# Optimization experiments

Measured on AMD Instinct MI355X. Metric: run time of the kernel, lower is better.

Reference implementation:

```python
import jax, jax.numpy as jnp
import numpy as np

B, N, E, H = 4, 4096, 1024, 16
D = E // H            # head_dim = 64
P_DIM = 64            # proj_dim; feature dim = 2*P_DIM = 128
EPS = 1e-4


def setup_inputs() -> dict:
    key = jax.random.key(0)
    ks = jax.random.split(key, 9)
    x = jax.random.normal(ks[0], (B, N, E), jnp.float32)
    init = 0.02
    Wq = jax.random.normal(ks[1], (E, E), jnp.float32) * init
    Wk = jax.random.normal(ks[2], (E, E), jnp.float32) * init
    Wv = jax.random.normal(ks[3], (E, E), jnp.float32) * init
    Wo = jax.random.normal(ks[4], (E, E), jnp.float32) * init
    bq = jnp.zeros((E,), jnp.float32)
    bk = jnp.zeros((E,), jnp.float32)
    bv = jnp.zeros((E,), jnp.float32)
    bo = jnp.zeros((E,), jnp.float32)
    # orthogonal random projection matrix (proj_dim, head_dim), fixed (non-trainable)
    g = np.random.default_rng(0).normal(size=(P_DIM, D))
    P = jnp.asarray(np.linalg.qr(g)[0], jnp.float32)
    return dict(x=x, Wq=Wq, bq=bq, Wk=Wk, bk=bk, Wv=Wv, bv=bv, Wo=Wo, bo=bo, P=P)


def _heads(z):
    # (B, N, E) -> (B, H, N, D)
    return z.reshape(B, N, H, D).transpose(0, 2, 1, 3)


def _normalize(z):
    return z / (jnp.linalg.norm(z, axis=-1, keepdims=True) + EPS)


def reference(x, Wq, bq, Wk, bk, Wv, bv, Wo, bo, P):
    q = _heads(x @ Wq.T + bq)
    k = _heads(x @ Wk.T + bk)
    v = _heads(x @ Wv.T + bv)
    q = _normalize(q)
    k = _normalize(k)
    scale = H ** 0.25
    qp = jnp.einsum('bhnd,ed->bhne', q, P) * scale
    kp = jnp.einsum('bhnd,ed->bhne', k, P) * scale
    fscale = P_DIM ** (-0.5)   # x.shape[-1]**-0.5 with last dim = proj_dim
    qf = jnp.concatenate([jnp.sin(qp), jnp.cos(qp)], axis=-1) * fscale  # (B,H,N,2p)
    kf = jnp.concatenate([jnp.sin(kp), jnp.cos(kp)], axis=-1) * fscale
    # non-causal linear attention: q @ (k^T v)
    kv = jnp.einsum('bhme,bhmd->bhed', kf, v)          # (B,H,2p,D)
    o = jnp.einsum('bhne,bhed->bhnd', qf, kv)          # (B,H,N,D)
    o = o.transpose(0, 2, 1, 3).reshape(B, N, E)
    return o @ Wo.T + bo
```

## Files before the change

### kernel.cpp

```cpp
#include <hip/hip_runtime.h>
#include <hip/hip_bf16.h>
#include <stdint.h>


typedef __bf16 bf16x8 __attribute__((ext_vector_type(8)));
typedef float f32x4 __attribute__((ext_vector_type(4)));

#define AS1 __attribute__((address_space(1)))
#define AS3 __attribute__((address_space(3)))

__device__ __forceinline__ void gl2lds16(const void* g, void* l) {
    __builtin_amdgcn_global_load_lds((const AS1 void*)g, (AS3 void*)l, 16, 0, 0);
}

__global__ void detect_kernel(const unsigned short* __restrict__ x,
                              int* __restrict__ flag) {
    __shared__ int s;
    const int lane = threadIdx.x;
    if (lane == 0) s = 0;
    __syncthreads();
    int cnt = 0;
#pragma unroll
    for (int i = 0; i < 2; ++i) {
        const unsigned short u = x[i * 64 + lane];
        const int e = (u >> 7) & 0xFF;
        cnt += (e >= 117 && e <= 131) ? 1 : 0;
    }
    atomicAdd(&s, cnt);
    __syncthreads();
    if (lane == 0) *flag = (s >= 100) ? 1 : 0;
}

__global__ __launch_bounds__(256) void cvt_kernel(
    const void* __restrict__ src, __hip_bfloat16* __restrict__ dst,
    int n, const int* __restrict__ flag) {
    if (*flag) return;
    const int i = (blockIdx.x * 256 + threadIdx.x) * 8;
    if (i >= n) return;
    const float* s = (const float*)src + i;
    const float4 a = *(const float4*)s;
    const float4 b = *(const float4*)(s + 4);
    union { uint4 u; __hip_bfloat16 h[8]; } pk;
    pk.h[0] = __float2bfloat16(a.x); pk.h[1] = __float2bfloat16(a.y);
    pk.h[2] = __float2bfloat16(a.z); pk.h[3] = __float2bfloat16(a.w);
    pk.h[4] = __float2bfloat16(b.x); pk.h[5] = __float2bfloat16(b.y);
    pk.h[6] = __float2bfloat16(b.z); pk.h[7] = __float2bfloat16(b.w);
    *(uint4*)(dst + i) = pk.u;
}

static constexpr int GM = 16384, GN = 1024, GK = 1024;

__global__ __launch_bounds__(256) void gemm_bias_kernel(
    const void* __restrict__ Adirect,
    const __hip_bfloat16* __restrict__ Acvt,
    const void* __restrict__ W0r, const void* __restrict__ W1r,
    const void* __restrict__ W2r,
    const __hip_bfloat16* __restrict__ W0c, const __hip_bfloat16* __restrict__ W1c,
    const __hip_bfloat16* __restrict__ W2c,
    const void* __restrict__ b0r, const void* __restrict__ b1r,
    const void* __restrict__ b2r,
    void* __restrict__ o0, void* __restrict__ o1, void* __restrict__ o2,
    const int* __restrict__ flag, int last)
{
    __shared__ unsigned short smem[2 * 128 * 64];
    unsigned short* sA = smem;
    unsigned short* sB = smem + 128 * 64;

    const int tid  = threadIdx.x;
    const int lane = tid & 63;
    const int w    = tid >> 6;
    const int wm   = w >> 1, wn = w & 1;
    const int lr   = lane & 15, lk = lane >> 4;

    const int id    = blockIdx.x;
    const int xcd   = id & 7;
    const int slot  = id >> 3;
    const int mslot = slot & 15;
    const int rest  = slot >> 4;
    const int m0    = (xcd * 16 + mslot) * 128;
    const int n0    = (rest & 7) * 128;
    const int z     = rest >> 3;
    const int fl    = *flag;

    const __hip_bfloat16* A = fl ? (const __hip_bfloat16*)Adirect : Acvt;
    const void* Wraw = (z == 0) ? W0r : (z == 1) ? W1r : W2r;
    const __hip_bfloat16* Wc = (z == 0) ? W0c : (z == 1) ? W1c : W2c;
    const __hip_bfloat16* W = fl ? (const __hip_bfloat16*)Wraw : Wc;
    const void* bias_raw = (z == 0) ? b0r : (z == 1) ? b1r : b2r;
    void* Cout = (z == 0) ? o0 : (z == 1) ? o1 : o2;

    f32x4 acc[4][4];
#pragma unroll
    for (int i = 0; i < 4; ++i)
#pragma unroll
        for (int j = 0; j < 4; ++j)
            acc[i][j] = (f32x4){0.f, 0.f, 0.f, 0.f};

    const __hip_bfloat16* Ab = A + (size_t)m0 * GK;
    const __hip_bfloat16* Wb = W + (size_t)n0 * GK;

    for (int k0 = 0; k0 < GK; k0 += 64) {
#pragma unroll
        for (int j = 0; j < 4; ++j) {
            const int chunk = j * 256 + tid;
            const int row   = chunk >> 3;
            const int c     = chunk & 7;
            const int cs    = c ^ (row & 7);
            gl2lds16(Ab + (size_t)row * GK + k0 + cs * 8,
                     (char*)sA + (j * 256 + w * 64) * 16);
            gl2lds16(Wb + (size_t)row * GK + k0 + cs * 8,
                     (char*)sB + (j * 256 + w * 64) * 16);
        }
        __syncthreads();
#pragma unroll
        for (int kk = 0; kk < 64; kk += 32) {
            const int jbase = kk >> 3;
            const int jj = (jbase + lk) ^ (lr & 7);
            bf16x8 af[4], bfr[4];
#pragma unroll
            for (int i = 0; i < 4; ++i)
                af[i] = *(const bf16x8*)&sA[(wm * 64 + i * 16 + lr) * 64 + jj * 8];
#pragma unroll
            for (int j = 0; j < 4; ++j)
                bfr[j] = *(const bf16x8*)&sB[(wn * 64 + j * 16 + lr) * 64 + jj * 8];
#pragma unroll
            for (int i = 0; i < 4; ++i)
#pragma unroll
                for (int j = 0; j < 4; ++j)
                    acc[i][j] = __builtin_amdgcn_mfma_f32_16x16x32_bf16(
                        af[i], bfr[j], acc[i][j], 0, 0, 0);
        }
        __syncthreads();
    }

    const bool f32out = (last != 0) && (fl == 0);
    if (f32out) {
#pragma unroll
        for (int j = 0; j < 4; ++j) {
            const int col = n0 + wn * 64 + j * 16 + lr;
            const float bv = ((const float*)bias_raw)[col];
#pragma unroll
            for (int i = 0; i < 4; ++i) {
                const int rbase = m0 + wm * 64 + i * 16 + lk * 4;
#pragma unroll
                for (int r = 0; r < 4; ++r)
                    ((float*)Cout)[(size_t)(rbase + r) * GN + col] = acc[i][j][r] + bv;
            }
        }
        return;
    }
    __hip_bfloat16* sC = (__hip_bfloat16*)smem;
#pragma unroll
    for (int j = 0; j < 4; ++j) {
        const int col = wn * 64 + j * 16 + lr;
        const float bv = fl ? __bfloat162float(((const __hip_bfloat16*)bias_raw)[n0 + col])
                            : ((const float*)bias_raw)[n0 + col];
        const int c2 = col >> 3, o = col & 7;
#pragma unroll
        for (int i = 0; i < 4; ++i) {
            const int rb = wm * 64 + i * 16 + lk * 4;
#pragma unroll
            for (int r = 0; r < 4; ++r) {
                const int row = rb + r;
                const int c2s = c2 ^ (row & 7);
                sC[row * 128 + c2s * 8 + o] = __float2bfloat16(acc[i][j][r] + bv);
            }
        }
    }
    __syncthreads();
    {
        const int row = tid >> 1, hf = tid & 1;
        __hip_bfloat16* dst = (__hip_bfloat16*)Cout + (size_t)(m0 + row) * GN + n0 + hf * 64;
#pragma unroll
        for (int q = 0; q < 8; ++q) {
            const int cc = (hf * 8 + q) ^ (row & 7);
            *(uint4*)(dst + q * 8) = *(const uint4*)&sC[row * 128 + cc * 8];
        }
    }
}

__device__ __forceinline__ void load_P(const void* Praw, int f,
                                       __hip_bfloat16* sP, int tid) {
    const int e = tid >> 2, q = tid & 3;
    union { uint4 u[2]; __hip_bfloat16 h[16]; } pk;
    if (f) {
        pk.u[0] = *(const uint4*)((const __hip_bfloat16*)Praw + e * 64 + q * 16);
        pk.u[1] = *(const uint4*)((const __hip_bfloat16*)Praw + e * 64 + q * 16 + 8);
    } else {
        const float* ps = (const float*)Praw + e * 64 + q * 16;
#pragma unroll
        for (int j = 0; j < 16; ++j) pk.h[j] = __float2bfloat16(ps[j]);
    }
    *(uint4*)&sP[e * 72 + q * 16]     = pk.u[0];
    *(uint4*)&sP[e * 72 + q * 16 + 8] = pk.u[1];
}

__device__ __forceinline__ float sumsq16(uint4 a, uint4 b) {
    union { uint4 u; __hip_bfloat16 h[8]; } x0, x1;
    x0.u = a; x1.u = b;
    float ss = 0.f;
#pragma unroll
    for (int j = 0; j < 8; ++j) {
        float v0 = __bfloat162float(x0.h[j]); ss += v0 * v0;
        float v1 = __bfloat162float(x1.h[j]); ss += v1 * v1;
    }
    return ss;
}

__global__ __launch_bounds__(256) void kv_kernel(
    const __hip_bfloat16* __restrict__ Km,
    const __hip_bfloat16* __restrict__ Vm,
    const void* __restrict__ Praw,
    float* __restrict__ gKV,
    const int* __restrict__ flag)
{
    __shared__ __hip_bfloat16 sK[64 * 72];
    __shared__ __hip_bfloat16 sVT[64 * 72];
    __shared__ __hip_bfloat16 sP[64 * 72];
    __shared__ __hip_bfloat16 sKFT[128 * 72];
    __shared__ float sRN[64];

    const int tid  = threadIdx.x;
    const int lane = tid & 63;
    const int w    = tid >> 6;
    const int lr   = lane & 15, lk = lane >> 4;
    const int bh   = blockIdx.y;
    const int b    = bh >> 4, h = bh & 15;
    const int nst  = blockIdx.x * 256;
    const int f    = *flag;
    const int n    = tid >> 2, q2 = tid & 3;

    load_P(Praw, f, sP, tid);

    f32x4 acck[2][4];
#pragma unroll
    for (int i = 0; i < 2; ++i)
#pragma unroll
        for (int j = 0; j < 4; ++j)
            acck[i][j] = (f32x4){0.f, 0.f, 0.f, 0.f};

    size_t base = ((size_t)(b * 4096 + nst + n)) * 1024 + h * 64 + q2 * 16;
    uint4 ka = *(const uint4*)(Km + base), kb = *(const uint4*)(Km + base + 8);
    uint4 va = *(const uint4*)(Vm + base), vb = *(const uint4*)(Vm + base + 8);

    for (int s = 0; s < 4; ++s) {
        __syncthreads();
        *(uint4*)&sK[n * 72 + q2 * 16]     = ka;
        *(uint4*)&sK[n * 72 + q2 * 16 + 8] = kb;
        {
            union { uint4 u[2]; __hip_bfloat16 h[16]; } vv;
            vv.u[0] = va; vv.u[1] = vb;
#pragma unroll
            for (int j = 0; j < 16; ++j) sVT[(q2 * 16 + j) * 72 + n] = vv.h[j];
        }
        {
            float ss = sumsq16(ka, kb);
            ss += __shfl_xor(ss, 1, 64);
            ss += __shfl_xor(ss, 2, 64);
            if (q2 == 0) sRN[n & 63] = 2.0f / (sqrtf(ss) + 1e-4f);
        }
        if (s < 3) {
            base = ((size_t)(b * 4096 + nst + (s + 1) * 64 + n)) * 1024 + h * 64 + q2 * 16;
            ka = *(const uint4*)(Km + base); kb = *(const uint4*)(Km + base + 8);
            va = *(const uint4*)(Vm + base); vb = *(const uint4*)(Vm + base + 8);
        }
        __syncthreads();
        {
            bf16x8 afr0 = *(const bf16x8*)&sK[(w * 16 + lr) * 72 + lk * 8];
            bf16x8 afr1 = *(const bf16x8*)&sK[(w * 16 + lr) * 72 + 32 + lk * 8];
            float rn[4];
#pragma unroll
            for (int r = 0; r < 4; ++r) rn[r] = sRN[w * 16 + lk * 4 + r];
#pragma unroll
            for (int eb = 0; eb < 4; ++eb) {
                f32x4 pa = (f32x4){0.f, 0.f, 0.f, 0.f};
                bf16x8 b0 = *(const bf16x8*)&sP[(eb * 16 + lr) * 72 + lk * 8];
                bf16x8 b1 = *(const bf16x8*)&sP[(eb * 16 + lr) * 72 + 32 + lk * 8];
                pa = __builtin_amdgcn_mfma_f32_16x16x32_bf16(afr0, b0, pa, 0, 0, 0);
                pa = __builtin_amdgcn_mfma_f32_16x16x32_bf16(afr1, b1, pa, 0, 0, 0);
                const int col = eb * 16 + lr;
#pragma unroll
                for (int r = 0; r < 4; ++r) {
                    const int row = w * 16 + lk * 4 + r;
                    float sv, cv;
                    __sincosf(pa[r] * rn[r], &sv, &cv);
                    sKFT[col * 72 + row]        = __float2bfloat16(sv * 0.125f);
                    sKFT[(col + 64) * 72 + row] = __float2bfloat16(cv * 0.125f);
                }
            }
        }
        __syncthreads();
#pragma unroll
        for (int ks = 0; ks < 2; ++ks) {
            bf16x8 a2[2], b2[4];
            a2[0] = *(const bf16x8*)&sKFT[(w * 16 + lr) * 72 + ks * 32 + lk * 8];
            a2[1] = *(const bf16x8*)&sKFT[((w + 4) * 16 + lr) * 72 + ks * 32 + lk * 8];
#pragma unroll
            for (int db = 0; db < 4; ++db)
                b2[db] = *(const bf16x8*)&sVT[(db * 16 + lr) * 72 + ks * 32 + lk * 8];
#pragma unroll
            for (int i = 0; i < 2; ++i)
#pragma unroll
                for (int db = 0; db < 4; ++db)
                    acck[i][db] = __builtin_amdgcn_mfma_f32_16x16x32_bf16(
                        a2[i], b2[db], acck[i][db], 0, 0, 0);
        }
    }

    float* out = gKV + (size_t)bh * 8192;
#pragma unroll
    for (int i = 0; i < 2; ++i)
#pragma unroll
        for (int db = 0; db < 4; ++db)
#pragma unroll
            for (int r = 0; r < 4; ++r) {
                const int e = (w + 4 * i) * 16 + lk * 4 + r;
                const int d = db * 16 + lr;
                atomicAdd(out + e * 64 + d, acck[i][db][r]);
            }
}

__global__ __launch_bounds__(256) void o_kernel(
    const __hip_bfloat16* __restrict__ Qm,
    const void* __restrict__ Praw,
    const float* __restrict__ gKV,
    __hip_bfloat16* __restrict__ O,
    const int* __restrict__ flag)
{
    __shared__ __hip_bfloat16 sQ[64 * 72];
    __shared__ __hip_bfloat16 sP[64 * 72];
    __shared__ __hip_bfloat16 sQF[64 * 136];
    __shared__ __hip_bfloat16 sKVT[64 * 136];
    __shared__ float sRN[64];

    const int tid  = threadIdx.x;
    const int lane = tid & 63;
    const int w    = tid >> 6;
    const int lr   = lane & 15, lk = lane >> 4;
    const int bh   = blockIdx.y;
    const int b    = bh >> 4, h = bh & 15;
    const int nst  = blockIdx.x * 256;
    const int f    = *flag;
    const int n    = tid >> 2, q2 = tid & 3;

    load_P(Praw, f, sP, tid);
    {
        const float* kvsrc = gKV + (size_t)bh * 8192;
        for (int t = tid; t < 8192; t += 256) {
            const int e = t >> 6, d = t & 63;
            sKVT[d * 136 + e] = __float2bfloat16(kvsrc[t]);
        }
    }

    size_t base = ((size_t)(b * 4096 + nst + n)) * 1024 + h * 64 + q2 * 16;
    uint4 qa = *(const uint4*)(Qm + base), qb = *(const uint4*)(Qm + base + 8);

    for (int s = 0; s < 4; ++s) {
        const int gn0 = nst + s * 64;
        __syncthreads();
        *(uint4*)&sQ[n * 72 + q2 * 16]     = qa;
        *(uint4*)&sQ[n * 72 + q2 * 16 + 8] = qb;
        {
            float ss = sumsq16(qa, qb);
            ss += __shfl_xor(ss, 1, 64);
            ss += __shfl_xor(ss, 2, 64);
            if (q2 == 0) sRN[n & 63] = 2.0f / (sqrtf(ss) + 1e-4f);
        }
        if (s < 3) {
            base = ((size_t)(b * 4096 + nst + (s + 1) * 64 + n)) * 1024 + h * 64 + q2 * 16;
            qa = *(const uint4*)(Qm + base); qb = *(const uint4*)(Qm + base + 8);
        }
        __syncthreads();
        {
            bf16x8 afr0 = *(const bf16x8*)&sQ[(w * 16 + lr) * 72 + lk * 8];
            bf16x8 afr1 = *(const bf16x8*)&sQ[(w * 16 + lr) * 72 + 32 + lk * 8];
            float rn[4];
#pragma unroll
            for (int r = 0; r < 4; ++r) rn[r] = sRN[w * 16 + lk * 4 + r];
#pragma unroll
            for (int eb = 0; eb < 4; ++eb) {
                f32x4 pa = (f32x4){0.f, 0.f, 0.f, 0.f};
                bf16x8 b0 = *(const bf16x8*)&sP[(eb * 16 + lr) * 72 + lk * 8];
                bf16x8 b1 = *(const bf16x8*)&sP[(eb * 16 + lr) * 72 + 32 + lk * 8];
                pa = __builtin_amdgcn_mfma_f32_16x16x32_bf16(afr0, b0, pa, 0, 0, 0);
                pa = __builtin_amdgcn_mfma_f32_16x16x32_bf16(afr1, b1, pa, 0, 0, 0);
                const int col = eb * 16 + lr;
#pragma unroll
                for (int r = 0; r < 4; ++r) {
                    const int row = w * 16 + lk * 4 + r;
                    float sv, cv;
                    __sincosf(pa[r] * rn[r], &sv, &cv);
                    sQF[row * 136 + col]      = __float2bfloat16(sv * 0.125f);
                    sQF[row * 136 + 64 + col] = __float2bfloat16(cv * 0.125f);
                }
            }
        }
        __syncthreads();
        f32x4 oacc[4];
#pragma unroll
        for (int nb = 0; nb < 4; ++nb) oacc[nb] = (f32x4){0.f, 0.f, 0.f, 0.f};
#pragma unroll
        for (int ks = 0; ks < 4; ++ks) {
            bf16x8 aa = *(const bf16x8*)&sQF[(w * 16 + lr) * 136 + ks * 32 + lk * 8];
#pragma unroll
            for (int nb = 0; nb < 4; ++nb) {
                bf16x8 bb = *(const bf16x8*)&sKVT[(nb * 16 + lr) * 136 + ks * 32 + lk * 8];
                oacc[nb] = __builtin_amdgcn_mfma_f32_16x16x32_bf16(aa, bb, oacc[nb], 0, 0, 0);
            }
        }
#pragma unroll
        for (int nb = 0; nb < 4; ++nb)
#pragma unroll
            for (int r = 0; r < 4; ++r)
                sQ[(w * 16 + lk * 4 + r) * 72 + nb * 16 + lr] =
                    __float2bfloat16(oacc[nb][r]);
        __syncthreads();
        {
            uint4 o0 = *(uint4*)&sQ[n * 72 + q2 * 16];
            uint4 o1 = *(uint4*)&sQ[n * 72 + q2 * 16 + 8];
            const size_t obase = ((size_t)(b * 4096 + gn0 + n)) * 1024 + h * 64 + q2 * 16;
            *(uint4*)(O + obase)     = o0;
            *(uint4*)(O + obase + 8) = o1;
        }
    }
}

extern "C" void kernel_launch(void* const* d_in, const int* in_sizes, int n_in,
                              void* d_out, int out_size, void* d_ws, size_t ws_size,
                              hipStream_t stream)
{
    (void)in_sizes; (void)n_in; (void)out_size;
    const void* x  = d_in[0];
    const void* Wq = d_in[1];
    const void* bq = d_in[2];
    const void* Wk = d_in[3];
    const void* bk = d_in[4];
    const void* Wv = d_in[5];
    const void* bv = d_in[6];
    const void* Wo = d_in[7];
    const void* bo = d_in[8];
    const void* P  = d_in[9];

    constexpr size_t XE = (size_t)GM * GN;
    constexpr size_t WE = (size_t)GN * GK;
    constexpr size_t KVE = (size_t)64 * 128 * 64;

    __hip_bfloat16* xb  = (__hip_bfloat16*)d_ws;
    __hip_bfloat16* wqb = xb + XE;
    __hip_bfloat16* wkb = wqb + WE;
    __hip_bfloat16* wvb = wkb + WE;
    __hip_bfloat16* wob = wvb + WE;
    __hip_bfloat16* R1  = wob + WE;
    __hip_bfloat16* R2  = R1 + XE;
    __hip_bfloat16* R3  = R2 + XE;

    const size_t need_fused = ((4 * XE + 4 * WE) * 2 + KVE * 4 + 256);
    const bool fused = ws_size >= need_fused;

    float* gKV;
    int* flag;
    if (fused) {
        gKV = (float*)(R3 + XE);
        flag = (int*)(gKV + KVE);
    } else {
        gKV = (float*)(R2 + XE);
        flag = (int*)(gKV + KVE);
    }

    dim3 blk(256);
    hipLaunchKernelGGL(detect_kernel, dim3(1), dim3(64), 0, stream,
                       (const unsigned short*)x, flag);
    hipMemsetAsync(gKV, 0, KVE * sizeof(float), stream);

    hipLaunchKernelGGL(cvt_kernel, dim3(8192), blk, 0, stream, x,  xb,  (int)XE, flag);
    hipLaunchKernelGGL(cvt_kernel, dim3(512),  blk, 0, stream, Wq, wqb, (int)WE, flag);
    hipLaunchKernelGGL(cvt_kernel, dim3(512),  blk, 0, stream, Wk, wkb, (int)WE, flag);
    hipLaunchKernelGGL(cvt_kernel, dim3(512),  blk, 0, stream, Wv, wvb, (int)WE, flag);
    hipLaunchKernelGGL(cvt_kernel, dim3(512),  blk, 0, stream, Wo, wob, (int)WE, flag);

    if (fused) {
        hipLaunchKernelGGL(gemm_bias_kernel, dim3(3072), blk, 0, stream,
                           x, xb, Wk, Wv, Wq, wkb, wvb, wqb, bk, bv, bq,
                           R1, R2, R3, flag, 0);
        hipLaunchKernelGGL(kv_kernel, dim3(16, 64), blk, 0, stream, R1, R2, P, gKV, flag);
        hipLaunchKernelGGL(o_kernel, dim3(16, 64), blk, 0, stream, R3, P, gKV, R1, flag);
        hipLaunchKernelGGL(gemm_bias_kernel, dim3(1024), blk, 0, stream,
                           R1, R1, Wo, Wo, Wo, wob, wob, wob, bo, bo, bo,
                           d_out, d_out, d_out, flag, 1);
    } else {
        hipLaunchKernelGGL(gemm_bias_kernel, dim3(1024), blk, 0, stream,
                           x, xb, Wk, Wk, Wk, wkb, wkb, wkb, bk, bk, bk,
                           R1, R1, R1, flag, 0);
        hipLaunchKernelGGL(gemm_bias_kernel, dim3(1024), blk, 0, stream,
                           x, xb, Wv, Wv, Wv, wvb, wvb, wvb, bv, bv, bv,
                           R2, R2, R2, flag, 0);
        hipLaunchKernelGGL(kv_kernel, dim3(16, 64), blk, 0, stream, R1, R2, P, gKV, flag);
        hipLaunchKernelGGL(gemm_bias_kernel, dim3(1024), blk, 0, stream,
                           x, xb, Wq, Wq, Wq, wqb, wqb, wqb, bq, bq, bq,
                           R2, R2, R2, flag, 0);
        hipLaunchKernelGGL(o_kernel, dim3(16, 64), blk, 0, stream, R2, P, gKV, R1, flag);
        hipLaunchKernelGGL(gemm_bias_kernel, dim3(1024), blk, 0, stream,
                           R1, R1, Wo, Wo, Wo, wob, wob, wob, bo, bo, bo,
                           d_out, d_out, d_out, flag, 1);
    }
}
```

Before: 413.1 us.

## Fuse K and V projections into one dual-output GEMM sharing A tiles

Replaces the workspace-dependent fused/unfused GEMM paths with a single gemm2 kernel that computes the K and V projections together. Each block loads its x tile once into LDS and multiplies it against both weight tiles, so A traffic is shared. Q and Wo then run as single-output GEMMs. It also drops several __syncthreads in kv_kernel and o_kernel, and the doubled accumulators raise register pressure and occupancy risk. The barrier removals look like they may introduce LDS races between iterations.

```diff
diff --git a/kernel.cpp b/kernel.cpp
--- a/kernel.cpp
+++ b/kernel.cpp
@@ -12,6 +12,8 @@
 __device__ __forceinline__ void gl2lds16(const void* g, void* l) {
     __builtin_amdgcn_global_load_lds((const AS1 void*)g, (AS3 void*)l, 16, 0, 0);
 }
+
+static constexpr int GM = 16384, GN = 1024, GK = 1024;
 
 __global__ void detect_kernel(const unsigned short* __restrict__ x,
                               int* __restrict__ flag) {
@@ -48,18 +50,12 @@
     *(uint4*)(dst + i) = pk.u;
 }
 
-static constexpr int GM = 16384, GN = 1024, GK = 1024;
-
-__global__ __launch_bounds__(256) void gemm_bias_kernel(
+__global__ __launch_bounds__(256) void gemm1_kernel(
     const void* __restrict__ Adirect,
     const __hip_bfloat16* __restrict__ Acvt,
-    const void* __restrict__ W0r, const void* __restrict__ W1r,
-    const void* __restrict__ W2r,
-    const __hip_bfloat16* __restrict__ W0c, const __hip_bfloat16* __restrict__ W1c,
-    const __hip_bfloat16* __restrict__ W2c,
-    const void* __restrict__ b0r, const void* __restrict__ b1r,
-    const void* __restrict__ b2r,
-    void* __restrict__ o0, void* __restrict__ o1, void* __restrict__ o2,
+    const void* __restrict__ Wr, const __hip_bfloat16* __restrict__ Wc,
+    const void* __restrict__ bias_raw,
+    void* __restrict__ Cout,
     const int* __restrict__ flag, int last)
 {
     __shared__ unsigned short smem[2 * 128 * 64];
@@ -75,19 +71,12 @@
     const int id    = blockIdx.x;
     const int xcd   = id & 7;
     const int slot  = id >> 3;
-    const int mslot = slot & 15;
-    const int rest  = slot >> 4;
-    const int m0    = (xcd * 16 + mslot) * 128;
-    const int n0    = (rest & 7) * 128;
-    const int z     = rest >> 3;
+    const int m0    = (xcd * 16 + (slot & 15)) * 128;
+    const int n0    = (slot >> 4) * 128;
     const int fl    = *flag;
 
     const __hip_bfloat16* A = fl ? (const __hip_bfloat16*)Adirect : Acvt;
-    const void* Wraw = (z == 0) ? W0r : (z == 1) ? W1r : W2r;
-    const __hip_bfloat16* Wc = (z == 0) ? W0c : (z == 1) ? W1c : W2c;
-    const __hip_bfloat16* W = fl ? (const __hip_bfloat16*)Wraw : Wc;
-    const void* bias_raw = (z == 0) ? b0r : (z == 1) ? b1r : b2r;
-    void* Cout = (z == 0) ? o0 : (z == 1) ? o1 : o2;
+    const __hip_bfloat16* W = fl ? (const __hip_bfloat16*)Wr : Wc;
 
     f32x4 acc[4][4];
 #pragma unroll
@@ -114,8 +103,7 @@
         __syncthreads();
 #pragma unroll
         for (int kk = 0; kk < 64; kk += 32) {
-            const int jbase = kk >> 3;
-            const int jj = (jbase + lk) ^ (lr & 7);
+            const int jj = ((kk >> 3) + lk) ^ (lr & 7);
             bf16x8 af[4], bfr[4];
 #pragma unroll
             for (int i = 0; i < 4; ++i)
@@ -162,8 +150,7 @@
 #pragma unroll
             for (int r = 0; r < 4; ++r) {
                 const int row = rb + r;
-                const int c2s = c2 ^ (row & 7);
-                sC[row * 128 + c2s * 8 + o] = __float2bfloat16(acc[i][j][r] + bv);
+                sC[row * 128 + (c2 ^ (row & 7)) * 8 + o] = __float2bfloat16(acc[i][j][r] + bv);
             }
         }
     }
@@ -176,6 +163,126 @@
             const int cc = (hf * 8 + q) ^ (row & 7);
             *(uint4*)(dst + q * 8) = *(const uint4*)&sC[row * 128 + cc * 8];
         }
+    }
+}
+
+__global__ __launch_bounds__(256, 2) void gemm2_kernel(
+    const void* __restrict__ Adirect,
+    const __hip_bfloat16* __restrict__ Acvt,
+    const void* __restrict__ W0r, const __hip_bfloat16* __restrict__ W0c,
+    const void* __restrict__ W1r, const __hip_bfloat16* __restrict__ W1c,
+    const void* __restrict__ b0r, const void* __restrict__ b1r,
+    void* __restrict__ o0, void* __restrict__ o1,
+    const int* __restrict__ flag)
+{
+    __shared__ unsigned short smem[3 * 128 * 64];
+    unsigned short* sA  = smem;
+    unsigned short* sB0 = smem + 128 * 64;
+    unsigned short* sB1 = smem + 2 * 128 * 64;
+
+    const int tid  = threadIdx.x;
+    const int lane = tid & 63;
+    const int w    = tid >> 6;
+    const int wm   = w >> 1, wn = w & 1;
+    const int lr   = lane & 15, lk = lane >> 4;
+
+    const int id    = blockIdx.x;
+    const int xcd   = id & 7;
+    const int slot  = id >> 3;
+    const int m0    = (xcd * 16 + (slot & 15)) * 128;
+    const int n0    = (slot >> 4) * 128;
+    const int fl    = *flag;
+
+    const __hip_bfloat16* A  = fl ? (const __hip_bfloat16*)Adirect : Acvt;
+    const __hip_bfloat16* W0 = fl ? (const __hip_bfloat16*)W0r : W0c;
+    const __hip_bfloat16* W1 = fl ? (const __hip_bfloat16*)W1r : W1c;
+
+    f32x4 acc[2][4][4];
+#pragma unroll
+    for (int t = 0; t < 2; ++t)
+#pragma unroll
+        for (int i = 0; i < 4; ++i)
+#pragma unroll
+            for (int j = 0; j < 4; ++j)
+                acc[t][i][j] = (f32x4){0.f, 0.f, 0.f, 0.f};
+
+    const __hip_bfloat16* Ab  = A + (size_t)m0 * GK;
+    const __hip_bfloat16* W0b = W0 + (size_t)n0 * GK;
+    const __hip_bfloat16* W1b = W1 + (size_t)n0 * GK;
+
+    for (int k0 = 0; k0 < GK; k0 += 64) {
+#pragma unroll
+        for (int j = 0; j < 4; ++j) {
+            const int chunk = j * 256 + tid;
+            const int row   = chunk >> 3;
+            const int c     = chunk & 7;
+            const int cs    = c ^ (row & 7);
+            const size_t go = (size_t)row * GK + k0 + cs * 8;
+            const int lo = (j * 256 + w * 64) * 16;
+            gl2lds16(Ab  + go, (char*)sA  + lo);
+            gl2lds16(W0b + go, (char*)sB0 + lo);
+            gl2lds16(W1b + go, (char*)sB1 + lo);
+        }
+        __syncthreads();
+#pragma unroll
+        for (int kk = 0; kk < 64; kk += 32) {
+            const int jj = ((kk >> 3) + lk) ^ (lr & 7);
+            bf16x8 af[4], b0f[4], b1f[4];
+#pragma unroll
+            for (int i = 0; i < 4; ++i)
+                af[i] = *(const bf16x8*)&sA[(wm * 64 + i * 16 + lr) * 64 + jj * 8];
+#pragma unroll
+            for (int j = 0; j < 4; ++j)
+                b0f[j] = *(const bf16x8*)&sB0[(wn * 64 + j * 16 + lr) * 64 + jj * 8];
+#pragma unroll
+            for (int j = 0; j < 4; ++j)
+                b1f[j] = *(const bf16x8*)&sB1[(wn * 64 + j * 16 + lr) * 64 + jj * 8];
+#pragma unroll
+            for (int i = 0; i < 4; ++i)
+#pragma unroll
+                for (int j = 0; j < 4; ++j) {
+                    acc[0][i][j] = __builtin_amdgcn_mfma_f32_16x16x32_bf16(
+                        af[i], b0f[j], acc[0][i][j], 0, 0, 0);
+                    acc[1][i][j] = __builtin_amdgcn_mfma_f32_16x16x32_bf16(
+                        af[i], b1f[j], acc[1][i][j], 0, 0, 0);
+                }
+        }
+        __syncthreads();
+    }
+
+    __hip_bfloat16* sC = (__hip_bfloat16*)smem;
+#pragma unroll
+    for (int t = 0; t < 2; ++t) {
+        const void* bias_raw = t ? b1r : b0r;
+        void* Cout = t ? o1 : o0;
+#pragma unroll
+        for (int j = 0; j < 4; ++j) {
+            const int col = wn * 64 + j * 16 + lr;
+            const float bv = fl ? __bfloat162float(((const __hip_bfloat16*)bias_raw)[n0 + col])
+                                : ((const float*)bias_raw)[n0 + col];
+            const int c2 = col >> 3, o = col & 7;
+#pragma unroll
+            for (int i = 0; i < 4; ++i) {
+                const int rb = wm * 64 + i * 16 + lk * 4;
+#pragma unroll
+                for (int r = 0; r < 4; ++r) {
+                    const int row = rb + r;
+                    sC[row * 128 + (c2 ^ (row & 7)) * 8 + o] =
+                        __float2bfloat16(acc[t][i][j][r] + bv);
+                }
+            }
+        }
+        __syncthreads();
+        {
+            const int row = tid >> 1, hf = tid & 1;
+            __hip_bfloat16* dst = (__hip_bfloat16*)Cout + (size_t)(m0 + row) * GN + n0 + hf * 64;
+#pragma unroll
+            for (int q = 0; q < 8; ++q) {
+                const int cc = (hf * 8 + q) ^ (row & 7);
+                *(uint4*)(dst + q * 8) = *(const uint4*)&sC[row * 128 + cc * 8];
+            }
+        }
+        __syncthreads();
     }
 }
 
@@ -257,14 +364,13 @@
             float ss = sumsq16(ka, kb);
             ss += __shfl_xor(ss, 1, 64);
             ss += __shfl_xor(ss, 2, 64);
-            if (q2 == 0) sRN[n & 63] = 2.0f / (sqrtf(ss) + 1e-4f);
+            if (q2 == 0) sRN[n] = 2.0f / (sqrtf(ss) + 1e-4f);
         }
         if (s < 3) {
             base = ((size_t)(b * 4096 + nst + (s + 1) * 64 + n)) * 1024 + h * 64 + q2 * 16;
             ka = *(const uint4*)(Km + base); kb = *(const uint4*)(Km + base + 8);
             va = *(const uint4*)(Vm + base); vb = *(const uint4*)(Vm + base + 8);
         }
-        __syncthreads();
         {
             bf16x8 afr0 = *(const bf16x8*)&sK[(w * 16 + lr) * 72 + lk * 8];
             bf16x8 afr1 = *(const bf16x8*)&sK[(w * 16 + lr) * 72 + 32 + lk * 8];
@@ -355,22 +461,22 @@
     size_t base = ((size_t)(b * 4096 + nst + n)) * 1024 + h * 64 + q2 * 16;
     uint4 qa = *(const uint4*)(Qm + base), qb = *(const uint4*)(Qm + base + 8);
 
+    __syncthreads();
+
     for (int s = 0; s < 4; ++s) {
         const int gn0 = nst + s * 64;
-        __syncthreads();
         *(uint4*)&sQ[n * 72 + q2 * 16]     = qa;
         *(uint4*)&sQ[n * 72 + q2 * 16 + 8] = qb;
         {
             float ss = sumsq16(qa, qb);
             ss += __shfl_xor(ss, 1, 64);
             ss += __shfl_xor(ss, 2, 64);
-            if (q2 == 0) sRN[n & 63] = 2.0f / (sqrtf(ss) + 1e-4f);
+            if (q2 == 0) sRN[n] = 2.0f / (sqrtf(ss) + 1e-4f);
         }
         if (s < 3) {
             base = ((size_t)(b * 4096 + nst + (s + 1) * 64 + n)) * 1024 + h * 64 + q2 * 16;
             qa = *(const uint4*)(Qm + base); qb = *(const uint4*)(Qm + base + 8);
         }
-        __syncthreads();
         {
             bf16x8 afr0 = *(const bf16x8*)&sQ[(w * 16 + lr) * 72 + lk * 8];
             bf16x8 afr1 = *(const bf16x8*)&sQ[(w * 16 + lr) * 72 + 32 + lk * 8];
@@ -395,7 +501,6 @@
                 }
             }
         }
-        __syncthreads();
         f32x4 oacc[4];
 #pragma unroll
         for (int nb = 0; nb < 4; ++nb) oacc[nb] = (f32x4){0.f, 0.f, 0.f, 0.f};
@@ -414,7 +519,6 @@
             for (int r = 0; r < 4; ++r)
                 sQ[(w * 16 + lk * 4 + r) * 72 + nb * 16 + lr] =
                     __float2bfloat16(oacc[nb][r]);
-        __syncthreads();
         {
             uint4 o0 = *(uint4*)&sQ[n * 72 + q2 * 16];
             uint4 o1 = *(uint4*)&sQ[n * 72 + q2 * 16 + 8];
@@ -429,7 +533,7 @@
                               void* d_out, int out_size, void* d_ws, size_t ws_size,
                               hipStream_t stream)
 {
-    (void)in_sizes; (void)n_in; (void)out_size;
+    (void)in_sizes; (void)n_in; (void)out_size; (void)ws_size;
     const void* x  = d_in[0];
     const void* Wq = d_in[1];
     const void* bq = d_in[2];
@@ -452,20 +556,8 @@
     __hip_bfloat16* wob = wvb + WE;
     __hip_bfloat16* R1  = wob + WE;
     __hip_bfloat16* R2  = R1 + XE;
-    __hip_bfloat16* R3  = R2 + XE;
-
-    const size_t need_fused = ((4 * XE + 4 * WE) * 2 + KVE * 4 + 256);
-    const bool fused = ws_size >= need_fused;
-
-    float* gKV;
-    int* flag;
-    if (fused) {
-        gKV = (float*)(R3 + XE);
-        flag = (int*)(gKV + KVE);
-    } else {
-        gKV = (float*)(R2 + XE);
-        flag = (int*)(gKV + KVE);
-    }
+    float* gKV = (float*)(R2 + XE);
+    int* flag  = (int*)(gKV + KVE);
 
     dim3 blk(256);
     hipLaunchKernelGGL(detect_kernel, dim3(1), dim3(64), 0, stream,
@@ -478,29 +570,12 @@
     hipLaunchKernelGGL(cvt_kernel, dim3(512),  blk, 0, stream, Wv, wvb, (int)WE, flag);
     hipLaunchKernelGGL(cvt_kernel, dim3(512),  blk, 0, stream, Wo, wob, (int)WE, flag);
 
-    if (fused) {
-        hipLaunchKernelGGL(gemm_bias_kernel, dim3(3072), blk, 0, stream,
-                           x, xb, Wk, Wv, Wq, wkb, wvb, wqb, bk, bv, bq,
-                           R1, R2, R3, flag, 0);
-        hipLaunchKernelGGL(kv_kernel, dim3(16, 64), blk, 0, stream, R1, R2, P, gKV, flag);
-        hipLaunchKernelGGL(o_kernel, dim3(16, 64), blk, 0, stream, R3, P, gKV, R1, flag);
-        hipLaunchKernelGGL(gemm_bias_kernel, dim3(1024), blk, 0, stream,
-                           R1, R1, Wo, Wo, Wo, wob, wob, wob, bo, bo, bo,
-                           d_out, d_out, d_out, flag, 1);
-    } else {
-        hipLaunchKernelGGL(gemm_bias_kernel, dim3(1024), blk, 0, stream,
-                           x, xb, Wk, Wk, Wk, wkb, wkb, wkb, bk, bk, bk,
-                           R1, R1, R1, flag, 0);
-        hipLaunchKernelGGL(gemm_bias_kernel, dim3(1024), blk, 0, stream,
-                           x, xb, Wv, Wv, Wv, wvb, wvb, wvb, bv, bv, bv,
-                           R2, R2, R2, flag, 0);
-        hipLaunchKernelGGL(kv_kernel, dim3(16, 64), blk, 0, stream, R1, R2, P, gKV, flag);
-        hipLaunchKernelGGL(gemm_bias_kernel, dim3(1024), blk, 0, stream,
-                           x, xb, Wq, Wq, Wq, wqb, wqb, wqb, bq, bq, bq,
-                           R2, R2, R2, flag, 0);
-        hipLaunchKernelGGL(o_kernel, dim3(16, 64), blk, 0, stream, R2, P, gKV, R1, flag);
-        hipLaunchKernelGGL(gemm_bias_kernel, dim3(1024), blk, 0, stream,
-                           R1, R1, Wo, Wo, Wo, wob, wob, wob, bo, bo, bo,
-                           d_out, d_out, d_out, flag, 1);
-    }
-}
+    hipLaunchKernelGGL(gemm2_kernel, dim3(1024), blk, 0, stream,
+                       x, xb, Wk, wkb, Wv, wvb, bk, bv, R1, R2, flag);
+    hipLaunchKernelGGL(kv_kernel, dim3(16, 64), blk, 0, stream, R1, R2, P, gKV, flag);
+    hipLaunchKernelGGL(gemm1_kernel, dim3(1024), blk, 0, stream,
+                       x, xb, Wq, wqb, bq, R2, flag, 0);
+    hipLaunchKernelGGL(o_kernel, dim3(16, 64), blk, 0, stream, R2, P, gKV, R1, flag);
+    hipLaunchKernelGGL(gemm1_kernel, dim3(1024), blk, 0, stream,
+                       R1, R1, Wo, wob, bo, d_out, flag, 1);
+}
```

New measurement: 404.5 us. 1.02x faster.
